# Kernel tuning notes

Hardware: AMD Instinct MI355X
Metric: run time of the kernel (lower is better)

The kernel has to match this reference:

```python
import jax, jax.numpy as jnp
import numpy as np

DIM = 1024
HEADS = 16
DIM_HEAD = 64
INNER = HEADS * DIM_HEAD  # 1024
SCALE = DIM_HEAD ** -0.5


def setup_inputs() -> dict:
    key = jax.random.key(0)
    ks = jax.random.split(key, 6)
    b, n = 4, 2048
    x = jax.random.normal(ks[0], (b, n, DIM), dtype=jnp.float32)
    gamma = jnp.ones((DIM,), dtype=jnp.float32)
    # weights stored (in, out); torch Linear computes x @ W.T with W (out, in)
    w_q = jax.random.normal(ks[1], (DIM, INNER), dtype=jnp.float32) * (DIM ** -0.5)
    w_kv = jax.random.normal(ks[2], (DIM, 2 * INNER), dtype=jnp.float32) * (DIM ** -0.5)
    w_out = jax.random.normal(ks[3], (INNER, DIM), dtype=jnp.float32) * (INNER ** -0.5)
    null_kv = jax.random.normal(ks[4], (2, HEADS, 1, DIM_HEAD), dtype=jnp.float32)
    return {"x": x, "gamma": gamma, "w_q": w_q, "w_kv": w_kv, "w_out": w_out, "null_kv": null_kv}


def _layer_norm(x, gamma):
    mu = jnp.mean(x, axis=-1, keepdims=True)
    var = jnp.var(x, axis=-1, keepdims=True)
    return (x - mu) * jax.lax.rsqrt(var + 1e-5) * gamma  # beta == 0


def reference(x, gamma, w_q, w_kv, w_out, null_kv):
    b, n, _ = x.shape
    xn = _layer_norm(x, gamma)
    q = xn @ w_q  # [b, n, inner]
    kv = xn @ w_kv
    k, v = jnp.split(kv, 2, axis=-1)
    q = q * SCALE

    def to_heads(t):
        return t.reshape(b, n, HEADS, DIM_HEAD).transpose(0, 2, 1, 3)  # b h n d

    q, k, v = map(to_heads, (q, k, v))
    nk = jnp.broadcast_to(null_kv[0][None], (b, HEADS, 1, DIM_HEAD))
    nv = jnp.broadcast_to(null_kv[1][None], (b, HEADS, 1, DIM_HEAD))
    k = jnp.concatenate([nk, k], axis=2)  # b h (n+1) d
    v = jnp.concatenate([nv, v], axis=2)
    sim = jnp.einsum('bhid,bhjd->bhij', q, k)
    attn = jax.nn.softmax(sim, axis=-1)
    out = jnp.einsum('bhij,bhjd->bhid', attn, v)
    out = out.transpose(0, 2, 1, 3).reshape(b, n, INNER)
    return out @ w_out
```

## Files before the change

kernel.cpp:

```cpp
#include <hip/hip_runtime.h>

typedef unsigned short ushort_t;
using f32x4   = __attribute__((ext_vector_type(4))) float;
using f32x16  = __attribute__((ext_vector_type(16))) float;
using bf16x8  = __attribute__((ext_vector_type(8))) __bf16;

typedef __attribute__((address_space(1))) const void gvoid_t;
typedef __attribute__((address_space(3))) void svoid_t;

union Frag {
    uint4    u4;
    bf16x8   b;
    ushort_t s[8];
};

__device__ __forceinline__ ushort_t f2bf(float f) {
    union { float f; unsigned u; } a; a.f = f;
    unsigned u = a.u;
    unsigned r = (u + 0x7fffu + ((u >> 16) & 1u)) >> 16;
    return (ushort_t)r;
}
__device__ __forceinline__ float bf2f(ushort_t b) {
    union { unsigned u; float f; } a; a.u = ((unsigned)b) << 16;
    return a.f;
}
__device__ __forceinline__ unsigned pack2bf(float lo, float hi) {
    union { __bf16 h[2]; unsigned u; } p;
    p.h[0] = (__bf16)lo;
    p.h[1] = (__bf16)hi;
    return p.u;
}
__device__ __forceinline__ float exp2_fast(float x) {
#if __has_builtin(__builtin_amdgcn_exp2f)
    return __builtin_amdgcn_exp2f(x);
#else
    return exp2f(x);
#endif
}
__device__ __forceinline__ void pl32swap(unsigned &x, unsigned &y) {
#if __has_builtin(__builtin_amdgcn_permlane32_swap)
    auto r = __builtin_amdgcn_permlane32_swap((int)x, (int)y, false, false);
    x = (unsigned)r[0]; y = (unsigned)r[1];
#else
    asm volatile("v_permlane32_swap_b32 %0, %1" : "+v"(x), "+v"(y));
#endif
}
__device__ __forceinline__ f32x16 mfma32(bf16x8 a, bf16x8 b, f32x16 c) {
    return __builtin_amdgcn_mfma_f32_32x32x16_bf16(a, b, c, 0, 0, 0);
}

#define QSCALE 0.18033688011112042f

__global__ __launch_bounds__(256)
void ln_kernel(const float* __restrict__ x, const float* __restrict__ gamma,
               ushort_t* __restrict__ xn)
{
    const int row = blockIdx.x;
    const int tid = threadIdx.x;
    const float4 v = *reinterpret_cast<const float4*>(x + (size_t)row * 1024 + tid * 4);

    float s = v.x + v.y + v.z + v.w;
    float q = v.x * v.x + v.y * v.y + v.z * v.z + v.w * v.w;
    #pragma unroll
    for (int off = 1; off <= 32; off <<= 1) {
        s += __shfl_xor(s, off);
        q += __shfl_xor(q, off);
    }
    __shared__ float ss[4], sq[4];
    if ((tid & 63) == 0) { ss[tid >> 6] = s; sq[tid >> 6] = q; }
    __syncthreads();
    const float S  = ss[0] + ss[1] + ss[2] + ss[3];
    const float Q  = sq[0] + sq[1] + sq[2] + sq[3];
    const float mu = S * (1.0f / 1024.0f);
    const float var = Q * (1.0f / 1024.0f) - mu * mu;
    const float rstd = rsqrtf(var + 1e-5f);

    const float4 gm = *reinterpret_cast<const float4*>(gamma + tid * 4);
    ushort4 o;
    o.x = f2bf((v.x - mu) * rstd * gm.x);
    o.y = f2bf((v.y - mu) * rstd * gm.y);
    o.z = f2bf((v.z - mu) * rstd * gm.z);
    o.w = f2bf((v.w - mu) * rstd * gm.w);
    *reinterpret_cast<ushort4*>(xn + (size_t)row * 1024 + tid * 4) = o;
}

__global__ __launch_bounds__(256)
void wt_kernel(const float* __restrict__ w, ushort_t* __restrict__ wt, int K, int N)
{
    __shared__ float tile[32][33];
    const int n0 = blockIdx.x * 32, k0 = blockIdx.y * 32;
    const int tx = threadIdx.x, ty = threadIdx.y;
    #pragma unroll
    for (int i = 0; i < 4; ++i) {
        int r = ty + i * 8;
        tile[r][tx] = w[(size_t)(k0 + r) * N + n0 + tx];
    }
    __syncthreads();
    #pragma unroll
    for (int i = 0; i < 4; ++i) {
        int r = ty + i * 8;
        wt[(size_t)(n0 + r) * K + k0 + tx] = f2bf(tile[tx][r]);
    }
}

template<int MODE>
__global__ __launch_bounds__(256)
void gemm_kernel(const ushort_t* __restrict__ A, const ushort_t* __restrict__ Bt,
                 ushort_t* __restrict__ o16a, ushort_t* __restrict__ o16b,
                 float* __restrict__ o32)
{
    __shared__ ushort_t ldsA[128 * 64];
    __shared__ ushort_t ldsB[128 * 64];

    const int tid = threadIdx.x;
    const int m0 = blockIdx.x * 128, n0 = blockIdx.y * 128;
    const int w = tid >> 6, l = tid & 63, g = l >> 4, c = l & 15;
    const int wm = w >> 1, wn = w & 1;

    const ushort_t* asrc[4];
    const ushort_t* bsrc[4];
    #pragma unroll
    for (int j = 0; j < 4; ++j) {
        const int gidx = j * 256 + tid;
        const int row = gidx >> 3;
        const int sl  = (gidx & 7) ^ (row & 7);
        asrc[j] = A  + (size_t)(m0 + row) * 1024 + sl * 8;
        bsrc[j] = Bt + (size_t)(n0 + row) * 1024 + sl * 8;
    }

    f32x4 acc[4][4];
    #pragma unroll
    for (int mi = 0; mi < 4; ++mi)
        #pragma unroll
        for (int ni = 0; ni < 4; ++ni)
            acc[mi][ni] = (f32x4){0.f, 0.f, 0.f, 0.f};

    const int swz = c & 7;

    for (int kt = 0; kt < 16; ++kt) {
        if (kt) __syncthreads();
        #pragma unroll
        for (int j = 0; j < 4; ++j) {
            __builtin_amdgcn_global_load_lds((gvoid_t*)(asrc[j] + kt * 64),
                                             (svoid_t*)(&ldsA[(j * 256 + tid) * 8]), 16, 0, 0);
            __builtin_amdgcn_global_load_lds((gvoid_t*)(bsrc[j] + kt * 64),
                                             (svoid_t*)(&ldsB[(j * 256 + tid) * 8]), 16, 0, 0);
        }
        __syncthreads();

        #pragma unroll
        for (int kk = 0; kk < 2; ++kk) {
            Frag af[4], bfr[4];
            #pragma unroll
            for (int mi = 0; mi < 4; ++mi)
                af[mi].u4 = *reinterpret_cast<const uint4*>(
                    &ldsA[(wm * 64 + mi * 16 + c) * 64 + ((((kk << 2) | g)) ^ swz) * 8]);
            #pragma unroll
            for (int ni = 0; ni < 4; ++ni)
                bfr[ni].u4 = *reinterpret_cast<const uint4*>(
                    &ldsB[(wn * 64 + ni * 16 + c) * 64 + ((((kk << 2) | g)) ^ swz) * 8]);
            #pragma unroll
            for (int mi = 0; mi < 4; ++mi)
                #pragma unroll
                for (int ni = 0; ni < 4; ++ni)
                    acc[mi][ni] = __builtin_amdgcn_mfma_f32_16x16x32_bf16(
                        af[mi].b, bfr[ni].b, acc[mi][ni], 0, 0, 0);
        }
    }

    #pragma unroll
    for (int mi = 0; mi < 4; ++mi) {
        const int mbase = m0 + wm * 64 + mi * 16 + g * 4;
        #pragma unroll
        for (int ni = 0; ni < 4; ++ni) {
            const int n = n0 + wn * 64 + ni * 16 + c;
            if (MODE == 0) {
                const int hh = n >> 6, d = n & 63;
                #pragma unroll
                for (int r = 0; r < 4; ++r) {
                    const int m = mbase + r;
                    const int b = m >> 11, tok = m & 2047;
                    o16a[(((size_t)b * 16 + hh) * 2048 + tok) * 64 + d] =
                        f2bf(acc[mi][ni][r] * QSCALE);
                }
            } else if (MODE == 1) {
                if (n < 1024) {
                    const int hh = n >> 6, d = n & 63;
                    #pragma unroll
                    for (int r = 0; r < 4; ++r) {
                        const int m = mbase + r;
                        const int b = m >> 11, tok = m & 2047;
                        o16a[(((size_t)b * 16 + hh) * 2048 + tok) * 64 + d] =
                            f2bf(acc[mi][ni][r]);
                    }
                } else {
                    const int nn = n - 1024;
                    const int hh = nn >> 6, d = nn & 63;
                    const int b = mbase >> 11, tok0 = mbase & 2047;
                    ushort4 pv;
                    pv.x = f2bf(acc[mi][ni][0]);
                    pv.y = f2bf(acc[mi][ni][1]);
                    pv.z = f2bf(acc[mi][ni][2]);
                    pv.w = f2bf(acc[mi][ni][3]);
                    *reinterpret_cast<ushort4*>(
                        o16b + (((size_t)b * 16 + hh) * 64 + d) * 2048 + tok0) = pv;
                }
            } else {
                #pragma unroll
                for (int r = 0; r < 4; ++r)
                    o32[(size_t)(mbase + r) * 1024 + n] = acc[mi][ni][r];
            }
        }
    }
}

__global__ __launch_bounds__(512)
void attn_kernel(const ushort_t* __restrict__ q, const ushort_t* __restrict__ k,
                 const ushort_t* __restrict__ vt, const float* __restrict__ nkv,
                 ushort_t* __restrict__ out)
{
    __shared__ ushort_t kvs[2][8192];

    const int tid = threadIdx.x;
    const int w = tid >> 6, l = tid & 63;
    const int qc = l & 31, hh = l >> 5;
    const int bh = blockIdx.x, qb = blockIdx.y, hd = bh & 15;

    const ushort_t* kb = k  + (size_t)bh * 2048 * 64;
    const ushort_t* vb = vt + (size_t)bh * 64 * 2048;

    const int srow = tid >> 3;
    const int ssl  = (tid & 7) ^ (srow & 7);
    const ushort_t* ksrc = kb + srow * 64 + ssl * 8;
    const ushort_t* vsrc = vb + srow * 2048 + ssl * 8;

    const ushort_t* qbase = q + ((size_t)bh * 2048 + qb * 256 + w * 32 + qc) * 64;
    Frag aq[4];
    #pragma unroll
    for (int dwin = 0; dwin < 4; ++dwin)
        aq[dwin].u4 = *reinterpret_cast<const uint4*>(qbase + dwin * 16 + hh * 8);

    float snull = 0.f;
    #pragma unroll
    for (int dwin = 0; dwin < 4; ++dwin) {
        const float4 n0 = *reinterpret_cast<const float4*>(nkv + hd * 64 + dwin * 16 + hh * 8);
        const float4 n1 = *reinterpret_cast<const float4*>(nkv + hd * 64 + dwin * 16 + hh * 8 + 4);
        snull += bf2f(aq[dwin].s[0]) * n0.x + bf2f(aq[dwin].s[1]) * n0.y
               + bf2f(aq[dwin].s[2]) * n0.z + bf2f(aq[dwin].s[3]) * n0.w;
        snull += bf2f(aq[dwin].s[4]) * n1.x + bf2f(aq[dwin].s[5]) * n1.y
               + bf2f(aq[dwin].s[6]) * n1.z + bf2f(aq[dwin].s[7]) * n1.w;
    }
    snull += __shfl_xor(snull, 32);

    float m_run  = snull;
    float l_part = (hh == 0) ? 1.f : 0.f;

    f32x16 acc[2];
    #pragma unroll
    for (int db = 0; db < 2; ++db)
        #pragma unroll
        for (int r = 0; r < 16; ++r)
            acc[db][r] = nkv[1024 + hd * 64 + db * 32 + (r & 3) + 8 * (r >> 2) + 4 * hh];

    const int swz = l & 7;

    __builtin_amdgcn_global_load_lds((gvoid_t*)(ksrc), (svoid_t*)(&kvs[0][tid * 8]), 16, 0, 0);
    __builtin_amdgcn_global_load_lds((gvoid_t*)(vsrc), (svoid_t*)(&kvs[0][4096 + tid * 8]), 16, 0, 0);
    __syncthreads();

    int cur = 0;
    for (int t = 0; t < 32; ++t) {
        if (t < 31) {
            __builtin_amdgcn_global_load_lds((gvoid_t*)(ksrc + (t + 1) * 4096),
                                             (svoid_t*)(&kvs[cur ^ 1][tid * 8]), 16, 0, 0);
            __builtin_amdgcn_global_load_lds((gvoid_t*)(vsrc + (t + 1) * 64),
                                             (svoid_t*)(&kvs[cur ^ 1][4096 + tid * 8]), 16, 0, 0);
        }
        const ushort_t* kbuf = &kvs[cur][0];
        const ushort_t* vbuf = &kvs[cur][4096];

        f32x16 st[2];
        __builtin_amdgcn_s_setprio(1);
        #pragma unroll
        for (int kvblk = 0; kvblk < 2; ++kvblk) {
            f32x16 z = {0.f,0.f,0.f,0.f, 0.f,0.f,0.f,0.f, 0.f,0.f,0.f,0.f, 0.f,0.f,0.f,0.f};
            #pragma unroll
            for (int dwin = 0; dwin < 4; ++dwin) {
                Frag kf;
                kf.u4 = *reinterpret_cast<const uint4*>(
                    &kbuf[(kvblk * 32 + (l & 31)) * 64 + (((dwin << 1) | hh) ^ swz) * 8]);
                z = mfma32(kf.b, aq[dwin].b, z);
            }
            st[kvblk] = z;
        }
        __builtin_amdgcn_s_setprio(0);

        float pm = st[0][0];
        #pragma unroll
        for (int r = 1; r < 16; ++r) pm = fmaxf(pm, st[0][r]);
        #pragma unroll
        for (int r = 0; r < 16; ++r) pm = fmaxf(pm, st[1][r]);
        pm = fmaxf(pm, __shfl_xor(pm, 32));

        if (__any(pm > m_run + 12.f)) {
            const float nm = fmaxf(m_run, pm);
            const float alpha = exp2_fast(m_run - nm);
            m_run = nm;
            l_part *= alpha;
            #pragma unroll
            for (int db = 0; db < 2; ++db)
                #pragma unroll
                for (int r = 0; r < 16; ++r)
                    acc[db][r] *= alpha;
        }

        float ts = 0.f;
        #pragma unroll
        for (int B = 0; B < 2; ++B)
            #pragma unroll
            for (int r = 0; r < 16; ++r) {
                st[B][r] = exp2_fast(st[B][r] - m_run);
                ts += st[B][r];
            }
        l_part += ts;

        Frag pb[2][2];
        #pragma unroll
        for (int B = 0; B < 2; ++B)
            #pragma unroll
            for (int kbv = 0; kbv < 2; ++kbv) {
                unsigned P = pack2bf(st[B][8 * kbv + 0], st[B][8 * kbv + 1]);
                unsigned Q = pack2bf(st[B][8 * kbv + 2], st[B][8 * kbv + 3]);
                unsigned R = pack2bf(st[B][8 * kbv + 4], st[B][8 * kbv + 5]);
                unsigned S = pack2bf(st[B][8 * kbv + 6], st[B][8 * kbv + 7]);
                pl32swap(P, R);
                pl32swap(Q, S);
                pb[B][kbv].u4.x = P;
                pb[B][kbv].u4.y = Q;
                pb[B][kbv].u4.z = R;
                pb[B][kbv].u4.w = S;
            }

        __builtin_amdgcn_s_setprio(1);
        #pragma unroll
        for (int db = 0; db < 2; ++db)
            #pragma unroll
            for (int B = 0; B < 2; ++B)
                #pragma unroll
                for (int kbv = 0; kbv < 2; ++kbv) {
                    Frag vf;
                    vf.u4 = *reinterpret_cast<const uint4*>(
                        &vbuf[(db * 32 + (l & 31)) * 64 + (((B << 2) | (kbv << 1) | hh) ^ swz) * 8]);
                    acc[db] = mfma32(vf.b, pb[B][kbv].b, acc[db]);
                }
        __builtin_amdgcn_s_setprio(0);

        __syncthreads();
        cur ^= 1;
    }

    l_part += __shfl_xor(l_part, 32);
    const float inv = 1.f / l_part;

    ushort_t* olds = &kvs[0][0];
    const int rowq = w * 32 + qc;
    #pragma unroll
    for (int db = 0; db < 2; ++db)
        #pragma unroll
        for (int rq = 0; rq < 4; ++rq) {
            uint2 ov;
            ov.x = pack2bf(acc[db][4 * rq + 0] * inv, acc[db][4 * rq + 1] * inv);
            ov.y = pack2bf(acc[db][4 * rq + 2] * inv, acc[db][4 * rq + 3] * inv);
            const int gL = db * 4 + rq;
            const int phys = gL ^ (qc & 7);
            *reinterpret_cast<uint2*>(&olds[(rowq * 8 + phys) * 8 + 4 * hh]) = ov;
        }
    __syncthreads();

    const size_t obase = ((size_t)(bh >> 4) * 2048 + qb * 256) * 1024 + hd * 64;
    #pragma unroll
    for (int p = 0; p < 4; ++p) {
        const int G = p * 512 + tid;
        const int row = G >> 3, sl = G & 7;
        const int phys = sl ^ (row & 7);
        uint4 v = *reinterpret_cast<const uint4*>(&olds[(row * 8 + phys) * 8]);
        *reinterpret_cast<uint4*>(out + obase + (size_t)row * 1024 + sl * 8) = v;
    }
}

extern "C" void kernel_launch(void* const* d_in, const int* in_sizes, int n_in,
                              void* d_out, int out_size, void* d_ws, size_t ws_size,
                              hipStream_t stream)
{
    (void)in_sizes; (void)n_in; (void)out_size; (void)ws_size;
    const float* x     = (const float*)d_in[0];
    const float* gamma = (const float*)d_in[1];
    const float* w_q   = (const float*)d_in[2];
    const float* w_kv  = (const float*)d_in[3];
    const float* w_out = (const float*)d_in[4];
    const float* nkv   = (const float*)d_in[5];
    float* out = (float*)d_out;

    char* ws = (char*)d_ws;
    ushort_t* xn   = (ushort_t*)(ws);
    ushort_t* wqT  = (ushort_t*)(ws + 16777216);
    ushort_t* wkvT = (ushort_t*)(ws + 18874368);
    ushort_t* woT  = (ushort_t*)(ws + 23068672);
    ushort_t* qh   = (ushort_t*)(ws + 25165824);
    ushort_t* kh   = (ushort_t*)(ws + 41943040);
    ushort_t* vtb  = (ushort_t*)(ws + 58720256);
    ushort_t* ao   = xn;

    ln_kernel<<<dim3(8192), dim3(256), 0, stream>>>(x, gamma, xn);
    wt_kernel<<<dim3(32, 32), dim3(32, 8), 0, stream>>>(w_q,  wqT, 1024, 1024);
    wt_kernel<<<dim3(64, 32), dim3(32, 8), 0, stream>>>(w_kv, wkvT, 1024, 2048);
    wt_kernel<<<dim3(32, 32), dim3(32, 8), 0, stream>>>(w_out, woT, 1024, 1024);

    gemm_kernel<0><<<dim3(64, 8),  dim3(256), 0, stream>>>(xn, wqT,  qh, nullptr, nullptr);
    gemm_kernel<1><<<dim3(64, 16), dim3(256), 0, stream>>>(xn, wkvT, kh, vtb, nullptr);

    attn_kernel<<<dim3(64, 8), dim3(512), 0, stream>>>(qh, kh, vtb, nkv, ao);

    gemm_kernel<2><<<dim3(64, 8), dim3(256), 0, stream>>>(ao, woT, nullptr, nullptr, out);
}
```

Before: 211.2 us.

## Double-buffer GEMM LDS tiles and fuse Q and KV projections into one launch

The GEMM main loop now uses two LDS buffers, so the global-to-LDS loads for the next K tile are issued while MFMAs run on the current tile, hiding load latency behind compute. The Q and KV weight transposes are written into one contiguous QKV weight buffer, and a single GEMM launch over 3072 output columns replaces the two separate projection launches, which gives a larger grid and one fewer launch. Shared memory per block doubles, which may lower occupancy. The epilogue routes columns to Q (scaled), K, or transposed V by column range.

```diff
diff --git a/kernel.cpp b/kernel.cpp
--- a/kernel.cpp
+++ b/kernel.cpp
@@ -103,14 +103,51 @@
     }
 }
 
+__device__ __forceinline__ void gemm_stage(const ushort_t* const* asrc,
+                                           const ushort_t* const* bsrc,
+                                           ushort_t* dA, ushort_t* dB,
+                                           int kt, int tid)
+{
+    #pragma unroll
+    for (int j = 0; j < 4; ++j) {
+        __builtin_amdgcn_global_load_lds((gvoid_t*)(asrc[j] + kt * 64),
+                                         (svoid_t*)(&dA[(j * 256 + tid) * 8]), 16, 0, 0);
+        __builtin_amdgcn_global_load_lds((gvoid_t*)(bsrc[j] + kt * 64),
+                                         (svoid_t*)(&dB[(j * 256 + tid) * 8]), 16, 0, 0);
+    }
+}
+__device__ __forceinline__ void gemm_comp(const ushort_t* bA, const ushort_t* bB,
+                                          f32x4 (&acc)[4][4],
+                                          int wm, int wn, int g, int c, int swz)
+{
+    #pragma unroll
+    for (int kk = 0; kk < 2; ++kk) {
+        Frag af[4], bfr[4];
+        #pragma unroll
+        for (int mi = 0; mi < 4; ++mi)
+            af[mi].u4 = *reinterpret_cast<const uint4*>(
+                &bA[(wm * 64 + mi * 16 + c) * 64 + ((((kk << 2) | g)) ^ swz) * 8]);
+        #pragma unroll
+        for (int ni = 0; ni < 4; ++ni)
+            bfr[ni].u4 = *reinterpret_cast<const uint4*>(
+                &bB[(wn * 64 + ni * 16 + c) * 64 + ((((kk << 2) | g)) ^ swz) * 8]);
+        #pragma unroll
+        for (int mi = 0; mi < 4; ++mi)
+            #pragma unroll
+            for (int ni = 0; ni < 4; ++ni)
+                acc[mi][ni] = __builtin_amdgcn_mfma_f32_16x16x32_bf16(
+                    af[mi].b, bfr[ni].b, acc[mi][ni], 0, 0, 0);
+    }
+}
+
 template<int MODE>
 __global__ __launch_bounds__(256)
 void gemm_kernel(const ushort_t* __restrict__ A, const ushort_t* __restrict__ Bt,
                  ushort_t* __restrict__ o16a, ushort_t* __restrict__ o16b,
                  float* __restrict__ o32)
 {
-    __shared__ ushort_t ldsA[128 * 64];
-    __shared__ ushort_t ldsB[128 * 64];
+    __shared__ ushort_t ldsA[2][128 * 64];
+    __shared__ ushort_t ldsB[2][128 * 64];
 
     const int tid = threadIdx.x;
     const int m0 = blockIdx.x * 128, n0 = blockIdx.y * 128;
@@ -137,35 +174,15 @@
 
     const int swz = c & 7;
 
-    for (int kt = 0; kt < 16; ++kt) {
-        if (kt) __syncthreads();
-        #pragma unroll
-        for (int j = 0; j < 4; ++j) {
-            __builtin_amdgcn_global_load_lds((gvoid_t*)(asrc[j] + kt * 64),
-                                             (svoid_t*)(&ldsA[(j * 256 + tid) * 8]), 16, 0, 0);
-            __builtin_amdgcn_global_load_lds((gvoid_t*)(bsrc[j] + kt * 64),
-                                             (svoid_t*)(&ldsB[(j * 256 + tid) * 8]), 16, 0, 0);
-        }
+    gemm_stage(asrc, bsrc, ldsA[0], ldsB[0], 0, tid);
+    #pragma unroll 1
+    for (int k2 = 0; k2 < 8; ++k2) {
         __syncthreads();
-
-        #pragma unroll
-        for (int kk = 0; kk < 2; ++kk) {
-            Frag af[4], bfr[4];
-            #pragma unroll
-            for (int mi = 0; mi < 4; ++mi)
-                af[mi].u4 = *reinterpret_cast<const uint4*>(
-                    &ldsA[(wm * 64 + mi * 16 + c) * 64 + ((((kk << 2) | g)) ^ swz) * 8]);
-            #pragma unroll
-            for (int ni = 0; ni < 4; ++ni)
-                bfr[ni].u4 = *reinterpret_cast<const uint4*>(
-                    &ldsB[(wn * 64 + ni * 16 + c) * 64 + ((((kk << 2) | g)) ^ swz) * 8]);
-            #pragma unroll
-            for (int mi = 0; mi < 4; ++mi)
-                #pragma unroll
-                for (int ni = 0; ni < 4; ++ni)
-                    acc[mi][ni] = __builtin_amdgcn_mfma_f32_16x16x32_bf16(
-                        af[mi].b, bfr[ni].b, acc[mi][ni], 0, 0, 0);
-        }
+        gemm_stage(asrc, bsrc, ldsA[1], ldsB[1], 2 * k2 + 1, tid);
+        gemm_comp(ldsA[0], ldsB[0], acc, wm, wn, g, c, swz);
+        __syncthreads();
+        if (k2 < 7) gemm_stage(asrc, bsrc, ldsA[0], ldsB[0], 2 * k2 + 2, tid);
+        gemm_comp(ldsA[1], ldsB[1], acc, wm, wn, g, c, swz);
     }
 
     #pragma unroll
@@ -175,26 +192,20 @@
         for (int ni = 0; ni < 4; ++ni) {
             const int n = n0 + wn * 64 + ni * 16 + c;
             if (MODE == 0) {
-                const int hh = n >> 6, d = n & 63;
-                #pragma unroll
-                for (int r = 0; r < 4; ++r) {
-                    const int m = mbase + r;
-                    const int b = m >> 11, tok = m & 2047;
-                    o16a[(((size_t)b * 16 + hh) * 2048 + tok) * 64 + d] =
-                        f2bf(acc[mi][ni][r] * QSCALE);
-                }
-            } else if (MODE == 1) {
-                if (n < 1024) {
-                    const int hh = n >> 6, d = n & 63;
+                if (n < 2048) {
+                    const int nn = n & 1023;
+                    const int hh = nn >> 6, d = nn & 63;
+                    const size_t base = (n < 1024) ? 0 : 8388608;
+                    const float scale = (n < 1024) ? QSCALE : 1.f;
                     #pragma unroll
                     for (int r = 0; r < 4; ++r) {
                         const int m = mbase + r;
                         const int b = m >> 11, tok = m & 2047;
-                        o16a[(((size_t)b * 16 + hh) * 2048 + tok) * 64 + d] =
-                            f2bf(acc[mi][ni][r]);
+                        o16a[base + (((size_t)b * 16 + hh) * 2048 + tok) * 64 + d] =
+                            f2bf(acc[mi][ni][r] * scale);
                     }
                 } else {
-                    const int nn = n - 1024;
+                    const int nn = n - 2048;
                     const int hh = nn >> 6, d = nn & 63;
                     const int b = mbase >> 11, tok0 = mbase & 2047;
                     ushort4 pv;
@@ -402,22 +413,20 @@
     float* out = (float*)d_out;
 
     char* ws = (char*)d_ws;
-    ushort_t* xn   = (ushort_t*)(ws);
-    ushort_t* wqT  = (ushort_t*)(ws + 16777216);
-    ushort_t* wkvT = (ushort_t*)(ws + 18874368);
-    ushort_t* woT  = (ushort_t*)(ws + 23068672);
-    ushort_t* qh   = (ushort_t*)(ws + 25165824);
-    ushort_t* kh   = (ushort_t*)(ws + 41943040);
-    ushort_t* vtb  = (ushort_t*)(ws + 58720256);
-    ushort_t* ao   = xn;
+    ushort_t* xn    = (ushort_t*)(ws);
+    ushort_t* wqkvT = (ushort_t*)(ws + 16777216);
+    ushort_t* woT   = (ushort_t*)(ws + 23068672);
+    ushort_t* qh    = (ushort_t*)(ws + 25165824);
+    ushort_t* vtb   = (ushort_t*)(ws + 58720256);
+    ushort_t* ao    = xn;
+    ushort_t* kh    = qh + 8388608;
 
     ln_kernel<<<dim3(8192), dim3(256), 0, stream>>>(x, gamma, xn);
-    wt_kernel<<<dim3(32, 32), dim3(32, 8), 0, stream>>>(w_q,  wqT, 1024, 1024);
-    wt_kernel<<<dim3(64, 32), dim3(32, 8), 0, stream>>>(w_kv, wkvT, 1024, 2048);
+    wt_kernel<<<dim3(32, 32), dim3(32, 8), 0, stream>>>(w_q,  wqkvT, 1024, 1024);
+    wt_kernel<<<dim3(64, 32), dim3(32, 8), 0, stream>>>(w_kv, wqkvT + 1048576, 1024, 2048);
     wt_kernel<<<dim3(32, 32), dim3(32, 8), 0, stream>>>(w_out, woT, 1024, 1024);
 
-    gemm_kernel<0><<<dim3(64, 8),  dim3(256), 0, stream>>>(xn, wqT,  qh, nullptr, nullptr);
-    gemm_kernel<1><<<dim3(64, 16), dim3(256), 0, stream>>>(xn, wkvT, kh, vtb, nullptr);
+    gemm_kernel<0><<<dim3(64, 24), dim3(256), 0, stream>>>(xn, wqkvT, qh, vtb, nullptr);
 
     attn_kernel<<<dim3(64, 8), dim3(512), 0, stream>>>(qh, kh, vtb, nkv, ao);
 
```

Result: no change. 208.1 us (-1.5%).
